# Optimization experiments

Measured on AMD Instinct MI355X. Metric: run time of the kernel, lower is better.

The kernel has to match this reference:

```python
import jax, jax.numpy as jnp
import numpy as np

CX, CY, FX, FY = 334.081, 169.808, 460.585, 460.268
EPS = 1e-07
T_ITER = 1000
MIN_POINTS = 5000
H, W, B = 360, 640, 2


def _point_cloud(depth_img):
    # depth_img: [C,H,W]; channel 2 if C==3 else channel 0
    depth = depth_img[2] if depth_img.shape[0] == 3 else depth_img[0]
    rows, cols = depth.shape
    c = jnp.arange(cols, dtype=depth.dtype)[None, :]
    r = jnp.arange(rows, dtype=depth.dtype)[:, None]
    valid = (depth > 0) & (depth < 65535)
    nanv = jnp.float32(jnp.nan)
    z = jnp.where(valid, depth / 1000.0, nanv)
    x = jnp.where(valid, z * (c - CX) / FX, nanv)
    y = jnp.where(valid, z * (r - CY) / FY, nanv)
    pcd = jnp.stack([x.ravel(), y.ravel(), z.ravel()], axis=1)  # [N,3]
    return pcd, valid.ravel()


def setup_inputs() -> dict:
    key = jax.random.key(0)
    k1, k2 = jax.random.split(key)
    fake = jax.random.uniform(k1, (B, 1, H, W), dtype=jnp.float32)
    real = jax.random.uniform(k2, (B, 1, H, W), dtype=jnp.float32)
    return {"fake": fake, "real": real, "epoch": 5, "show_image": 0}


def _forward(fake, real, epoch):
    real_pcd, vr = _point_cloud(real[0])
    fake_pcd, vf = _point_cloud(fake[0])
    real_pcd = real_pcd * 1000.0
    fake_pcd = fake_pcd * 1000.0
    # pcd[pcd==0] = eps  (NaN==0 is False, NaNs preserved)
    real_pcd = jnp.where(real_pcd == 0, EPS, real_pcd)
    fake_pcd = jnp.where(fake_pcd == 0, EPS, fake_pcd)

    # combined validity mask (real-valid then fake-valid filtering chain)
    m = vr & vf
    cnt = jnp.maximum(jnp.sum(m), 1)

    def sel(v, fill):
        return jnp.where(m, v, fill)

    def mrmse(a, b):
        d = sel(a, 0.0) - sel(b, 0.0)
        return jnp.sqrt(jnp.sum(d * d) / cnt)

    lossX = mrmse(real_pcd[:, 0], fake_pcd[:, 0])
    lossY = mrmse(real_pcd[:, 1], fake_pcd[:, 1])
    lossZ = mrmse(real_pcd[:, 2], fake_pcd[:, 2])
    dlog = jnp.log(jnp.abs(sel(real_pcd[:, 2], 1.0))) - jnp.log(jnp.abs(sel(fake_pcd[:, 2], 1.0)))
    RMSE_log = 10000.0 * jnp.sqrt(jnp.sum(jnp.where(m, dlog * dlog, 0.0)) / cnt)
    loss17 = RMSE_log * jnp.abs(10.0 * (3.0 - jnp.exp(lossX) - jnp.exp(lossY) - jnp.exp(lossZ)))

    # ---- batched RANSAC plane fit on normalized fake cloud ----
    nan_cloud = jnp.where(jnp.isnan(fake_pcd), 0.0, fake_pcd)
    pts = nan_cloud / jnp.max(nan_cloud)  # [N,3]
    N = pts.shape[0]
    thresh = jnp.maximum(jnp.float32(0.025 - 0.001 * epoch), jnp.float32(0.005))

    rkey = jax.random.key(42)
    idx = jax.random.randint(rkey, (T_ITER, 3), 0, N)  # 3 sample points per trial
    p = pts[idx]  # [T,3,3]
    vA = p[:, 1] - p[:, 0]
    vB = p[:, 2] - p[:, 0]
    nrm = jnp.cross(vA, vB)
    nrm = nrm / jnp.linalg.norm(nrm, axis=1, keepdims=True)  # unit normals [T,3]
    kk = -jnp.sum(nrm * p[:, 1], axis=1)  # plane offsets [T]
    dist = pts @ nrm.T + kk[None, :]  # [N,T], |n|=1 so no extra divide
    inl = jnp.abs(dist) <= thresh  # [N,T]
    counts = jnp.sum(inl, axis=0)  # [T]
    # keep first trial with strictly-largest count among counts > minPoints
    score = jnp.where(counts > MIN_POINTS, counts, -1)
    best = jnp.argmax(score)
    a, b, c, d = nrm[best, 0], nrm[best, 1], nrm[best, 2], kk[best]
    inlier_mask = inl[:, best]  # [N]

    # translation/rotation were built via torch.tensor(...) -> detached in torch
    trans = jax.lax.stop_gradient(jnp.stack([jnp.zeros(()), jnp.zeros(()), d / c]))
    n2 = a * a + b * b + c * c
    cos_t = c / jnp.sqrt(n2)
    sin_t = jnp.sqrt((a * a + b * b) / n2)
    sab = jnp.sqrt(a * a + b * b)
    u1 = b / sab
    u2 = -a / sab
    R = jnp.stack([
        jnp.stack([cos_t + u1 * u1 * (1 - cos_t), u1 * u2 * (1 - cos_t), u2 * sin_t]),
        jnp.stack([u1 * u2 * (1 - cos_t), cos_t + u2 * u2 * (1 - cos_t), -u1 * sin_t]),
        jnp.stack([-u2 * sin_t, u1 * sin_t, cos_t]),
    ])
    Rt = jax.lax.stop_gradient(R).T  # torch transposes before matmul

    plane_pts = pts + trans
    zc = (plane_pts @ Rt)[:, 2]  # rotated z for all points; inliers selected by mask
    icnt = jnp.maximum(jnp.sum(inlier_mask), 1)
    zmax = jnp.max(jnp.where(inlier_mask, zc, -jnp.inf))
    zmin = jnp.min(jnp.where(inlier_mask, zc, jnp.inf))
    below = jnp.sum(jnp.where(inlier_mask, jnp.abs(zc - zmax), 0.0)) / icnt
    above = jnp.sum(jnp.where(inlier_mask, jnp.abs(zc - zmin), 0.0)) / icnt
    above = jnp.where(above == 0, jnp.float32(1e-07), above)
    plane_mean_dist_grad = 1000.0 * (above + below)

    loss_curv = loss17 + plane_mean_dist_grad
    delta = jnp.stack([RMSE_log, lossX, lossY, lossZ, plane_mean_dist_grad, loss17])
    return delta, loss_curv


def reference(fake, real, epoch, show_image):
    del show_image  # unused in the loss math
    return _forward(fake, real, epoch)
```

## Files before the change

kernel.cpp:

```cpp
#include <hip/hip_runtime.h>

namespace {

typedef float v2f __attribute__((ext_vector_type(2)));

constexpr int kW = 640;
constexpr int kN = 230400;
constexpr unsigned kSpan = 230400u;
constexpr int kB1 = 900;
constexpr int kB3 = 1024;
constexpr int kPPB3 = 225;
constexpr int kB5 = 900;
constexpr unsigned kPoison = 0xAAAAAAAAu;

struct __align__(16) Acc {
  double lossX, lossY, lossZ, rmse_log, loss17;
  float maxv;
  unsigned selkey;
};

constexpr size_t kOffAcc     = 0;
constexpr size_t kOffC1      = 256;
constexpr size_t kOffC3      = 320;
constexpr size_t kOffC5      = 384;
constexpr size_t kOffPlanes  = 512;
constexpr size_t kOffSP      = 512 + 16384;
constexpr size_t kOffZP      = kOffSP + 43200;
constexpr size_t kOffPartial = kOffZP + 28800;
constexpr size_t kOffPts     = kOffPartial + (size_t)kB3 * 256 * 4;

__device__ __forceinline__ void ast64(unsigned long long* p, unsigned long long v) {
  __hip_atomic_store(p, v, __ATOMIC_RELAXED, __HIP_MEMORY_SCOPE_AGENT);
}
__device__ __forceinline__ unsigned long long ald64(const unsigned long long* p) {
  return __hip_atomic_load(p, __ATOMIC_RELAXED, __HIP_MEMORY_SCOPE_AGENT);
}
__device__ __forceinline__ void ast32(unsigned* p, unsigned v) {
  __hip_atomic_store(p, v, __ATOMIC_RELAXED, __HIP_MEMORY_SCOPE_AGENT);
}
__device__ __forceinline__ unsigned ald32(const unsigned* p) {
  return __hip_atomic_load(p, __ATOMIC_RELAXED, __HIP_MEMORY_SCOPE_AGENT);
}

__device__ __forceinline__ unsigned rotl32(unsigned v, int r) {
  return (v << r) | (v >> (32 - r));
}

__device__ __forceinline__ void threefry(unsigned c0, unsigned c1,
                                         unsigned& o0, unsigned& o1) {
  const unsigned ks0 = 0u, ks1 = 42u, ks2 = 0x1BD11BDAu ^ 0u ^ 42u;
  unsigned x0 = c0 + ks0, x1 = c1 + ks1;
#define TFR(r) { x0 += x1; x1 = rotl32(x1, (r)); x1 ^= x0; }
  TFR(13) TFR(15) TFR(26) TFR(6)
  x0 += ks1; x1 += ks2 + 1u;
  TFR(17) TFR(29) TFR(16) TFR(24)
  x0 += ks2; x1 += ks0 + 2u;
  TFR(13) TFR(15) TFR(26) TFR(6)
  x0 += ks0; x1 += ks1 + 3u;
  TFR(17) TFR(29) TFR(16) TFR(24)
  x0 += ks1; x1 += ks2 + 4u;
  TFR(13) TFR(15) TFR(26) TFR(6)
  x0 += ks2; x1 += ks0 + 5u;
#undef TFR
  o0 = x0; o1 = x1;
}

__device__ __forceinline__ void pix_coords(float d, int row, int col, bool& valid,
                                           float& x, float& y, float& z) {
  valid = (d > 0.0f) && (d < 65535.0f);
  float z0 = d / 1000.0f;
  float x0 = z0 * ((float)col - 334.081f) / 460.585f;
  float y0 = z0 * ((float)row - 169.808f) / 460.268f;
  x = x0 * 1000.0f;
  y = y0 * 1000.0f;
  z = z0 * 1000.0f;
  if (x == 0.0f) x = 1e-7f;
  if (y == 0.0f) y = 1e-7f;
  if (z == 0.0f) z = 1e-7f;
}

__device__ __forceinline__ void make_pt(float d, int row, int col, float maxv,
                                        float& x, float& y, float& z) {
  bool v; float a, b, c;
  pix_coords(d, row, col, v, a, b, c);
  x = (v ? a : 0.f) / maxv;
  y = (v ? b : 0.f) / maxv;
  z = (v ? c : 0.f) / maxv;
}

__device__ __forceinline__ float get_thresh(int ep) {
  return (float)fmax(0.025 - 0.001 * (double)ep, 0.005);
}

__global__ __launch_bounds__(256) void k_stats(const float* __restrict__ fake,
                                               const float* __restrict__ real,
                                               float* __restrict__ out,
                                               char* __restrict__ ws) {
  Acc* acc = (Acc*)(ws + kOffAcc);
  unsigned* ctr = (unsigned*)(ws + kOffC1);
  float4* planes = (float4*)(ws + kOffPlanes);
  unsigned long long* sp = (unsigned long long*)(ws + kOffSP);
  float4* ptsraw = (float4*)(ws + kOffPts);

  const int b = blockIdx.x, t = threadIdx.x;
  const int lane = t & 63, wid = t >> 6;

  __shared__ double sD0[4], sD1[4], sD2[4], sD3[4];
  __shared__ int sI0[4];
  __shared__ float sF0[4];
  __shared__ unsigned sArr;
  __shared__ float sMaxv;

  {
    int i = b * 256 + t;
    int row = i / kW, col = i - row * kW;
    bool vr, vf; float rx, ry, rz, fx, fy, fz;
    pix_coords(real[i], row, col, vr, rx, ry, rz);
    pix_coords(fake[i], row, col, vf, fx, fy, fz);
    ptsraw[i] = make_float4(vf ? fx : 0.f, vf ? fy : 0.f, vf ? fz : 0.f, 0.f);
    double dx2 = 0, dy2 = 0, dz2 = 0, dl2 = 0; int cc = 0;
    if (vr && vf) {
      float ddx = rx - fx, ddy = ry - fy, ddz = rz - fz;
      dx2 = (double)ddx * (double)ddx;
      dy2 = (double)ddy * (double)ddy;
      dz2 = (double)ddz * (double)ddz;
      double dl = log(fabs((double)rz)) - log(fabs((double)fz));
      dl2 = dl * dl;
      cc = 1;
    }
    float mx = vf ? fmaxf(fmaxf(fx, fy), fz) : 0.0f;
    for (int o = 32; o; o >>= 1) {
      dx2 += __shfl_down(dx2, o); dy2 += __shfl_down(dy2, o);
      dz2 += __shfl_down(dz2, o); dl2 += __shfl_down(dl2, o);
      cc += __shfl_down(cc, o);
      mx = fmaxf(mx, __shfl_down(mx, o));
    }
    if (lane == 0) { sD0[wid]=dx2; sD1[wid]=dy2; sD2[wid]=dz2; sD3[wid]=dl2;
                     sI0[wid]=cc; sF0[wid]=mx; }
    __syncthreads();
    if (t == 0) {
      unsigned long long* e = sp + (size_t)b * 6;
      ast64(e + 0, __double_as_longlong(sD0[0]+sD0[1]+sD0[2]+sD0[3]));
      ast64(e + 1, __double_as_longlong(sD1[0]+sD1[1]+sD1[2]+sD1[3]));
      ast64(e + 2, __double_as_longlong(sD2[0]+sD2[1]+sD2[2]+sD2[3]));
      ast64(e + 3, __double_as_longlong(sD3[0]+sD3[1]+sD3[2]+sD3[3]));
      ast64(e + 4, (unsigned long long)(sI0[0]+sI0[1]+sI0[2]+sI0[3]));
      float bm = fmaxf(fmaxf(sF0[0], sF0[1]), fmaxf(sF0[2], sF0[3]));
      ast64(e + 5, (unsigned long long)__float_as_uint(bm));
    }
  }
  __syncthreads();
  if (t == 0)
    sArr = __hip_atomic_fetch_add(ctr, 1u, __ATOMIC_RELAXED, __HIP_MEMORY_SCOPE_AGENT);
  __syncthreads();
  if (sArr != kPoison + (unsigned)(kB1 - 1)) return;

  {
    double gx = 0, gy = 0, gz = 0, gl = 0; int gc = 0; float gm = 0.f;
    for (int r = t; r < kB1; r += 256) {
      const unsigned long long* e = sp + (size_t)r * 6;
      gx += __longlong_as_double(ald64(e + 0));
      gy += __longlong_as_double(ald64(e + 1));
      gz += __longlong_as_double(ald64(e + 2));
      gl += __longlong_as_double(ald64(e + 3));
      gc += (int)ald64(e + 4);
      gm = fmaxf(gm, __uint_as_float((unsigned)ald64(e + 5)));
    }
    for (int o = 32; o; o >>= 1) {
      gx += __shfl_down(gx, o); gy += __shfl_down(gy, o);
      gz += __shfl_down(gz, o); gl += __shfl_down(gl, o);
      gc += __shfl_down(gc, o);
      gm = fmaxf(gm, __shfl_down(gm, o));
    }
    if (lane == 0) { sD0[wid]=gx; sD1[wid]=gy; sD2[wid]=gz; sD3[wid]=gl;
                     sI0[wid]=gc; sF0[wid]=gm; }
    __syncthreads();
    if (t == 0) {
      double SX = sD0[0]+sD0[1]+sD0[2]+sD0[3];
      double SY = sD1[0]+sD1[1]+sD1[2]+sD1[3];
      double SZ = sD2[0]+sD2[1]+sD2[2]+sD2[3];
      double SL = sD3[0]+sD3[1]+sD3[2]+sD3[3];
      int CN = sI0[0]+sI0[1]+sI0[2]+sI0[3];
      float MX = fmaxf(fmaxf(sF0[0], sF0[1]), fmaxf(sF0[2], sF0[3]));
      double cntd = (CN > 0) ? (double)CN : 1.0;
      double lossX = sqrt(SX / cntd);
      double lossY = sqrt(SY / cntd);
      double lossZ = sqrt(SZ / cntd);
      double rmse_log = 10000.0 * sqrt(SL / cntd);
      double loss17 = rmse_log * fabs(10.0 * (3.0 - exp(lossX) - exp(lossY) - exp(lossZ)));
      acc->lossX = lossX; acc->lossY = lossY; acc->lossZ = lossZ;
      acc->rmse_log = rmse_log; acc->loss17 = loss17;
      acc->maxv = MX;
      acc->selkey = 0u;
      out[0] = (float)rmse_log;
      out[1] = (float)lossX;
      out[2] = (float)lossY;
      out[3] = (float)lossZ;
      out[5] = (float)loss17;
      sMaxv = MX;
    }
    __syncthreads();
  }
  {
    float maxv = sMaxv;
#pragma unroll
    for (int j = 0; j < 4; j++) {
      int pid = t * 4 + j;
      if (pid < 1000) {
        float px[3], py[3], pz[3];
#pragma unroll
        for (int v = 0; v < 3; v++) {
          unsigned p = 3u * (unsigned)pid + (unsigned)v;
          unsigned o0, o1;
          threefry(p, p + 3000u, o0, o1);
          unsigned idx = o1 % kSpan;
          int row = (int)(idx / kW), col = (int)idx - row * kW;
          make_pt(fake[idx], row, col, maxv, px[v], py[v], pz[v]);
        }
        float ax = px[1]-px[0], ay = py[1]-py[0], az = pz[1]-pz[0];
        float bx = px[2]-px[0], by = py[2]-py[0], bz = pz[2]-pz[0];
        float nx = ay*bz - az*by;
        float ny = az*bx - ax*bz;
        float nz = ax*by - ay*bx;
        float nn = sqrtf(nx*nx + ny*ny + nz*nz);
        nx /= nn; ny /= nn; nz /= nn;
        float kk = -(nx*px[1] + ny*py[1] + nz*pz[1]);
        planes[pid] = make_float4(nx, ny, nz, kk);
      } else {
        planes[pid] = make_float4(0.f, 0.f, 0.f, 3e38f);
      }
    }
  }
}

__global__ __launch_bounds__(256) void k_count(const int* __restrict__ epoch,
                                               char* __restrict__ ws) {
  Acc* acc = (Acc*)(ws + kOffAcc);
  unsigned* ctr = (unsigned*)(ws + kOffC3);
  const float4* planes = (const float4*)(ws + kOffPlanes);
  unsigned* partial = (unsigned*)(ws + kOffPartial);
  const float4* ptsraw = (const float4*)(ws + kOffPts);

  const int b = blockIdx.x, t = threadIdx.x;
  const float th = get_thresh(*epoch);
  const float maxv = acc->maxv;

  __shared__ float4 sPts[kPPB3];
  __shared__ uint4 sAcc[16][16];
  __shared__ unsigned sArr;

  if (t < kPPB3) {
    float4 r = ptsraw[b * kPPB3 + t];
    sPts[t] = make_float4(r.x / maxv, r.y / maxv, r.z / maxv, 0.f);
  }
  float4 p0 = planes[t * 4 + 0], p1 = planes[t * 4 + 1];
  float4 p2 = planes[t * 4 + 2], p3 = planes[t * 4 + 3];
  v2f Ax = {p0.x, p1.x}, Ay = {p0.y, p1.y}, Az = {p0.z, p1.z}, Aw = {p0.w, p1.w};
  v2f Bx = {p2.x, p3.x}, By = {p2.y, p3.y}, Bz = {p2.z, p3.z}, Bw = {p2.w, p3.w};
  __syncthreads();

  int c0 = 0, c1 = 0, c2 = 0, c3 = 0;
#pragma unroll 5
  for (int s = 0; s < kPPB3; ++s) {
    float4 q = sPts[s];
    v2f qx = {q.x, q.x}, qy = {q.y, q.y}, qz = {q.z, q.z};
    v2f dA = __builtin_elementwise_fma(qx, Ax,
             __builtin_elementwise_fma(qy, Ay,
             __builtin_elementwise_fma(qz, Az, Aw)));
    v2f dB = __builtin_elementwise_fma(qx, Bx,
             __builtin_elementwise_fma(qy, By,
             __builtin_elementwise_fma(qz, Bz, Bw)));
    c0 += (fabsf(dA.x) <= th) ? 1 : 0;
    c1 += (fabsf(dA.y) <= th) ? 1 : 0;
    c2 += (fabsf(dB.x) <= th) ? 1 : 0;
    c3 += (fabsf(dB.y) <= th) ? 1 : 0;
  }
  ast32(&partial[b * 256 + t],
        (unsigned)c0 | ((unsigned)c1 << 8) | ((unsigned)c2 << 16) | ((unsigned)c3 << 24));

  __syncthreads();
  if (t == 0)
    sArr = __hip_atomic_fetch_add(ctr, 1u, __ATOMIC_RELAXED, __HIP_MEMORY_SCOPE_AGENT);
  __syncthreads();
  unsigned ret = sArr;
  if (ret < kPoison + (unsigned)(kB3 - 16)) return;

  int r = (int)(ret - (kPoison + (unsigned)(kB3 - 16)));
  if (t == 0) {
    while (ald32(ctr) != kPoison + (unsigned)kB3) __builtin_amdgcn_s_sleep(2);
  }
  __syncthreads();

  int owner = r * 16 + (t & 15);
  int chunk = t >> 4;
  unsigned s0 = 0, s1 = 0, s2 = 0, s3 = 0;
  for (int row = chunk * 64; row < chunk * 64 + 64; ++row) {
    unsigned v = ald32(&partial[row * 256 + owner]);
    s0 += v & 0xFFu; s1 += (v >> 8) & 0xFFu;
    s2 += (v >> 16) & 0xFFu; s3 += (v >> 24) & 0xFFu;
  }
  sAcc[t & 15][chunk] = make_uint4(s0, s1, s2, s3);
  __syncthreads();

  unsigned mykey = 0u;
  if (t < 16) {
    unsigned t0 = 0, t1 = 0, t2 = 0, t3 = 0;
    for (int j = 0; j < 16; ++j) {
      uint4 v = sAcc[t][j];
      t0 += v.x; t1 += v.y; t2 += v.z; t3 += v.w;
    }
    unsigned tot[4] = {t0, t1, t2, t3};
    int pbase = (r * 16 + t) * 4;
#pragma unroll
    for (int k = 0; k < 4; ++k) {
      int p = pbase + k;
      if (p < 1000) {
        int score = ((int)tot[k] > 5000) ? (int)tot[k] : -1;
        unsigned key = ((unsigned)(score + 2) << 10) | (unsigned)(1023 - p);
        mykey = key > mykey ? key : mykey;
      }
    }
  }
  for (int o = 32; o; o >>= 1) {
    unsigned other = __shfl_down(mykey, o);
    mykey = other > mykey ? other : mykey;
  }
  if (t == 0) atomicMax(&acc->selkey, mykey);
}

__global__ __launch_bounds__(256) void k_zc(const int* __restrict__ epoch,
                                            float* __restrict__ out,
                                            char* __restrict__ ws) {
  Acc* acc = (Acc*)(ws + kOffAcc);
  unsigned* ctr = (unsigned*)(ws + kOffC5);
  const float4* planes = (const float4*)(ws + kOffPlanes);
  unsigned long long* zp = (unsigned long long*)(ws + kOffZP);
  const float4* ptsraw = (const float4*)(ws + kOffPts);

  const int b = blockIdx.x, t = threadIdx.x;
  const int lane = t & 63, wid = t >> 6;
  const float th = get_thresh(*epoch);
  const float maxv = acc->maxv;

  int best = 1023 - (int)(acc->selkey & 1023u);
  float4 pl = planes[best];
  const float a = pl.x, bb = pl.y, c = pl.z, d = pl.w;
  float n2 = a * a + bb * bb + c * c;
  float cos_t = c / sqrtf(n2);
  float sin_t = sqrtf((a * a + bb * bb) / n2);
  float sab = sqrtf(a * a + bb * bb);
  float u1 = bb / sab, u2 = -a / sab;
  const float r0 = -u2 * sin_t, r1 = u1 * sin_t, r2 = cos_t, tz = d / c;

  __shared__ double sD0[4];
  __shared__ int sI0[4];
  __shared__ float sF0[4], sF1[4];
  __shared__ unsigned sArr;

  double sz = 0.0; int ic = 0; float zmx = -INFINITY, zmn = -INFINITY;
  {
    float4 rw = ptsraw[b * 256 + t];
    float qx = rw.x / maxv, qy = rw.y / maxv, qz = rw.z / maxv;
    float dist = fmaf(qx, a, fmaf(qy, bb, fmaf(qz, c, d)));
    if (fabsf(dist) <= th) {
      float zc = fmaf(qx, r0, fmaf(qy, r1, (qz + tz) * r2));
      sz = (double)zc; ic = 1; zmx = zc; zmn = -zc;
    }
  }
  for (int o = 32; o; o >>= 1) {
    sz += __shfl_down(sz, o); ic += __shfl_down(ic, o);
    zmx = fmaxf(zmx, __shfl_down(zmx, o));
    zmn = fmaxf(zmn, __shfl_down(zmn, o));
  }
  if (lane == 0) { sD0[wid] = sz; sI0[wid] = ic; sF0[wid] = zmx; sF1[wid] = zmn; }
  __syncthreads();
  if (t == 0) {
    unsigned long long* e = zp + (size_t)b * 4;
    ast64(e + 0, __double_as_longlong(sD0[0]+sD0[1]+sD0[2]+sD0[3]));
    ast64(e + 1, (unsigned long long)(sI0[0]+sI0[1]+sI0[2]+sI0[3]));
    float bmx = fmaxf(fmaxf(sF0[0], sF0[1]), fmaxf(sF0[2], sF0[3]));
    float bmn = fmaxf(fmaxf(sF1[0], sF1[1]), fmaxf(sF1[2], sF1[3]));
    ast64(e + 2, (unsigned long long)__float_as_uint(bmx) |
                 ((unsigned long long)__float_as_uint(bmn) << 32));
  }
  __syncthreads();
  if (t == 0)
    sArr = __hip_atomic_fetch_add(ctr, 1u, __ATOMIC_RELAXED, __HIP_MEMORY_SCOPE_AGENT);
  __syncthreads();
  if (sArr != kPoison + (unsigned)(kB5 - 1)) return;

  {
    double gs = 0.0; int gi = 0; float gmx = -INFINITY, gmn = -INFINITY;
    for (int r = t; r < kB5; r += 256) {
      const unsigned long long* e = zp + (size_t)r * 4;
      gs += __longlong_as_double(ald64(e + 0));
      gi += (int)ald64(e + 1);
      unsigned long long mm = ald64(e + 2);
      gmx = fmaxf(gmx, __uint_as_float((unsigned)(mm & 0xFFFFFFFFu)));
      gmn = fmaxf(gmn, __uint_as_float((unsigned)(mm >> 32)));
    }
    for (int o = 32; o; o >>= 1) {
      gs += __shfl_down(gs, o); gi += __shfl_down(gi, o);
      gmx = fmaxf(gmx, __shfl_down(gmx, o));
      gmn = fmaxf(gmn, __shfl_down(gmn, o));
    }
    if (lane == 0) { sD0[wid] = gs; sI0[wid] = gi; sF0[wid] = gmx; sF1[wid] = gmn; }
    __syncthreads();
    if (t == 0) {
      double S = sD0[0]+sD0[1]+sD0[2]+sD0[3];
      int IC = sI0[0]+sI0[1]+sI0[2]+sI0[3];
      float MX = fmaxf(fmaxf(sF0[0], sF0[1]), fmaxf(sF0[2], sF0[3]));
      float MN = fmaxf(fmaxf(sF1[0], sF1[1]), fmaxf(sF1[2], sF1[3]));
      double below = 0.0, above = 0.0;
      if (IC > 0) {
        double icd = (double)IC;
        double mean = S / icd;
        below = (double)MX - mean;
        above = mean - (double)(-MN);
      }
      if (above == 0.0) above = 1e-7;
      double pmdg = 1000.0 * (above + below);
      out[4] = (float)pmdg;
      out[6] = (float)(acc->loss17 + pmdg);
    }
  }
}

}

extern "C" void kernel_launch(void* const* d_in, const int* in_sizes, int n_in,
                              void* d_out, int out_size, void* d_ws, size_t ws_size,
                              hipStream_t stream) {
  (void)in_sizes; (void)n_in; (void)out_size; (void)ws_size;
  const float* fake = (const float*)d_in[0];
  const float* real = (const float*)d_in[1];
  const int* epoch = (const int*)d_in[2];
  float* out = (float*)d_out;
  char* ws = (char*)d_ws;

  k_stats<<<kB1, 256, 0, stream>>>(fake, real, out, ws);
  k_count<<<kB3, 256, 0, stream>>>(epoch, ws);
  k_zc<<<kB5, 256, 0, stream>>>(epoch, out, ws);
}
```

Baseline: 136.9 us.

## Fuse three kernels into one cooperative persistent kernel with spin-wait grid barriers

Replaces the three launches (stats, inlier count, z-range) with a single cooperative kernel of 512 blocks. Each block keeps its 450 points in registers and shared memory across phases instead of writing and re-reading a global point buffer. Phases are joined by atomic counters and spin-wait flags. The goal is to remove launch gaps and global round-trips. In exchange it adds serialized waits on one block building the planes and risks deadlock if the blocks are not all co-resident.

```diff
diff --git a/kernel.cpp b/kernel.cpp
--- a/kernel.cpp
+++ b/kernel.cpp
@@ -7,27 +7,23 @@
 constexpr int kW = 640;
 constexpr int kN = 230400;
 constexpr unsigned kSpan = 230400u;
-constexpr int kB1 = 900;
-constexpr int kB3 = 1024;
-constexpr int kPPB3 = 225;
-constexpr int kB5 = 900;
+constexpr int kB = 512;
+constexpr int kPPB = 450;
 constexpr unsigned kPoison = 0xAAAAAAAAu;
 
-struct __align__(16) Acc {
-  double lossX, lossY, lossZ, rmse_log, loss17;
-  float maxv;
-  unsigned selkey;
-};
-
-constexpr size_t kOffAcc     = 0;
-constexpr size_t kOffC1      = 256;
-constexpr size_t kOffC3      = 320;
-constexpr size_t kOffC5      = 384;
-constexpr size_t kOffPlanes  = 512;
-constexpr size_t kOffSP      = 512 + 16384;
-constexpr size_t kOffZP      = kOffSP + 43200;
-constexpr size_t kOffPartial = kOffZP + 28800;
-constexpr size_t kOffPts     = kOffPartial + (size_t)kB3 * 256 * 4;
+constexpr size_t kOffMaxv   = 0;
+constexpr size_t kOffLoss17 = 8;
+constexpr size_t kOffC1     = 128;
+constexpr size_t kOffF1     = 192;
+constexpr size_t kOffC2     = 256;
+constexpr size_t kOffC2b    = 320;
+constexpr size_t kOffF2     = 384;
+constexpr size_t kOffC3     = 448;
+constexpr size_t kOffSel    = 512;
+constexpr size_t kOffPlanes = 1024;
+constexpr size_t kOffSP     = 1024 + 16384;
+constexpr size_t kOffZP     = kOffSP + 24576;
+constexpr size_t kOffPart   = 131072;
 
 __device__ __forceinline__ void ast64(unsigned long long* p, unsigned long long v) {
   __hip_atomic_store(p, v, __ATOMIC_RELAXED, __HIP_MEMORY_SCOPE_AGENT);
@@ -38,10 +34,6 @@
 __device__ __forceinline__ void ast32(unsigned* p, unsigned v) {
   __hip_atomic_store(p, v, __ATOMIC_RELAXED, __HIP_MEMORY_SCOPE_AGENT);
 }
-__device__ __forceinline__ unsigned ald32(const unsigned* p) {
-  return __hip_atomic_load(p, __ATOMIC_RELAXED, __HIP_MEMORY_SCOPE_AGENT);
-}
-
 __device__ __forceinline__ unsigned rotl32(unsigned v, int r) {
   return (v << r) | (v >> (32 - r));
 }
@@ -92,43 +84,76 @@
   return (float)fmax(0.025 - 0.001 * (double)ep, 0.005);
 }
 
-__global__ __launch_bounds__(256) void k_stats(const float* __restrict__ fake,
-                                               const float* __restrict__ real,
-                                               float* __restrict__ out,
-                                               char* __restrict__ ws) {
-  Acc* acc = (Acc*)(ws + kOffAcc);
-  unsigned* ctr = (unsigned*)(ws + kOffC1);
-  float4* planes = (float4*)(ws + kOffPlanes);
+__global__ __launch_bounds__(256, 2) void k_all(const float* __restrict__ fake,
+                                                const float* __restrict__ real,
+                                                const int* __restrict__ epoch,
+                                                float* __restrict__ out,
+                                                char* __restrict__ ws) {
+  unsigned long long* wMaxv = (unsigned long long*)(ws + kOffMaxv);
+  unsigned long long* wL17 = (unsigned long long*)(ws + kOffLoss17);
+  unsigned* wC1 = (unsigned*)(ws + kOffC1);
+  unsigned* wF1 = (unsigned*)(ws + kOffF1);
+  unsigned* wC2 = (unsigned*)(ws + kOffC2);
+  unsigned* wC2b = (unsigned*)(ws + kOffC2b);
+  unsigned* wF2 = (unsigned*)(ws + kOffF2);
+  unsigned* wC3 = (unsigned*)(ws + kOffC3);
+  unsigned* wSel = (unsigned*)(ws + kOffSel);
+  unsigned long long* planes = (unsigned long long*)(ws + kOffPlanes);
   unsigned long long* sp = (unsigned long long*)(ws + kOffSP);
-  float4* ptsraw = (float4*)(ws + kOffPts);
+  unsigned long long* zp = (unsigned long long*)(ws + kOffZP);
+  unsigned long long* part = (unsigned long long*)(ws + kOffPart);
 
   const int b = blockIdx.x, t = threadIdx.x;
   const int lane = t & 63, wid = t >> 6;
-
+  const float th = get_thresh(*epoch);
+
+  __shared__ float4 sPts[kPPB];
+  __shared__ uint4 sAcc[16][16];
   __shared__ double sD0[4], sD1[4], sD2[4], sD3[4];
   __shared__ int sI0[4];
-  __shared__ float sF0[4];
-  __shared__ unsigned sArr;
-  __shared__ float sMaxv;
-
+  __shared__ float sF0[4], sF1s[4];
+  __shared__ unsigned sU;
+
+  float p0x, p0y, p0z, p1x = 0.f, p1y = 0.f, p1z = 0.f;
+  const bool has2 = (t < kPPB - 256);
   {
-    int i = b * 256 + t;
-    int row = i / kW, col = i - row * kW;
-    bool vr, vf; float rx, ry, rz, fx, fy, fz;
-    pix_coords(real[i], row, col, vr, rx, ry, rz);
-    pix_coords(fake[i], row, col, vf, fx, fy, fz);
-    ptsraw[i] = make_float4(vf ? fx : 0.f, vf ? fy : 0.f, vf ? fz : 0.f, 0.f);
-    double dx2 = 0, dy2 = 0, dz2 = 0, dl2 = 0; int cc = 0;
-    if (vr && vf) {
-      float ddx = rx - fx, ddy = ry - fy, ddz = rz - fz;
-      dx2 = (double)ddx * (double)ddx;
-      dy2 = (double)ddy * (double)ddy;
-      dz2 = (double)ddz * (double)ddz;
-      double dl = log(fabs((double)rz)) - log(fabs((double)fz));
-      dl2 = dl * dl;
-      cc = 1;
-    }
-    float mx = vf ? fmaxf(fmaxf(fx, fy), fz) : 0.0f;
+    double dx2 = 0, dy2 = 0, dz2 = 0, dl2 = 0; int cc = 0; float mx = 0.f;
+    {
+      int i = b * kPPB + t;
+      int row = i / kW, col = i - row * kW;
+      bool vr, vf; float rx, ry, rz, fx, fy, fz;
+      pix_coords(real[i], row, col, vr, rx, ry, rz);
+      pix_coords(fake[i], row, col, vf, fx, fy, fz);
+      p0x = vf ? fx : 0.f; p0y = vf ? fy : 0.f; p0z = vf ? fz : 0.f;
+      if (vr && vf) {
+        float ddx = rx - fx, ddy = ry - fy, ddz = rz - fz;
+        dx2 += (double)ddx * (double)ddx;
+        dy2 += (double)ddy * (double)ddy;
+        dz2 += (double)ddz * (double)ddz;
+        double dl = log(fabs((double)rz)) - log(fabs((double)fz));
+        dl2 += dl * dl;
+        cc++;
+      }
+      if (vf) mx = fmaxf(mx, fmaxf(fmaxf(fx, fy), fz));
+    }
+    if (has2) {
+      int i = b * kPPB + t + 256;
+      int row = i / kW, col = i - row * kW;
+      bool vr, vf; float rx, ry, rz, fx, fy, fz;
+      pix_coords(real[i], row, col, vr, rx, ry, rz);
+      pix_coords(fake[i], row, col, vf, fx, fy, fz);
+      p1x = vf ? fx : 0.f; p1y = vf ? fy : 0.f; p1z = vf ? fz : 0.f;
+      if (vr && vf) {
+        float ddx = rx - fx, ddy = ry - fy, ddz = rz - fz;
+        dx2 += (double)ddx * (double)ddx;
+        dy2 += (double)ddy * (double)ddy;
+        dz2 += (double)ddz * (double)ddz;
+        double dl = log(fabs((double)rz)) - log(fabs((double)fz));
+        dl2 += dl * dl;
+        cc++;
+      }
+      if (vf) mx = fmaxf(mx, fmaxf(fmaxf(fx, fy), fz));
+    }
     for (int o = 32; o; o >>= 1) {
       dx2 += __shfl_down(dx2, o); dy2 += __shfl_down(dy2, o);
       dz2 += __shfl_down(dz2, o); dl2 += __shfl_down(dl2, o);
@@ -151,13 +176,12 @@
   }
   __syncthreads();
   if (t == 0)
-    sArr = __hip_atomic_fetch_add(ctr, 1u, __ATOMIC_RELAXED, __HIP_MEMORY_SCOPE_AGENT);
-  __syncthreads();
-  if (sArr != kPoison + (unsigned)(kB1 - 1)) return;
-
-  {
+    sU = __hip_atomic_fetch_add(wC1, 1u, __ATOMIC_ACQ_REL, __HIP_MEMORY_SCOPE_AGENT);
+  __syncthreads();
+
+  if (sU == kPoison + (unsigned)(kB - 1)) {
     double gx = 0, gy = 0, gz = 0, gl = 0; int gc = 0; float gm = 0.f;
-    for (int r = t; r < kB1; r += 256) {
+    for (int r = t; r < kB; r += 256) {
       const unsigned long long* e = sp + (size_t)r * 6;
       gx += __longlong_as_double(ald64(e + 0));
       gy += __longlong_as_double(ald64(e + 1));
@@ -175,6 +199,7 @@
     if (lane == 0) { sD0[wid]=gx; sD1[wid]=gy; sD2[wid]=gz; sD3[wid]=gl;
                      sI0[wid]=gc; sF0[wid]=gm; }
     __syncthreads();
+    __shared__ float sMaxv;
     if (t == 0) {
       double SX = sD0[0]+sD0[1]+sD0[2]+sD0[3];
       double SY = sD1[0]+sD1[1]+sD1[2]+sD1[3];
@@ -188,80 +213,84 @@
       double lossZ = sqrt(SZ / cntd);
       double rmse_log = 10000.0 * sqrt(SL / cntd);
       double loss17 = rmse_log * fabs(10.0 * (3.0 - exp(lossX) - exp(lossY) - exp(lossZ)));
-      acc->lossX = lossX; acc->lossY = lossY; acc->lossZ = lossZ;
-      acc->rmse_log = rmse_log; acc->loss17 = loss17;
-      acc->maxv = MX;
-      acc->selkey = 0u;
       out[0] = (float)rmse_log;
       out[1] = (float)lossX;
       out[2] = (float)lossY;
       out[3] = (float)lossZ;
       out[5] = (float)loss17;
+      ast64(wMaxv, (unsigned long long)__float_as_uint(MX));
+      ast64(wL17, __double_as_longlong(loss17));
+      ast32(wSel, 0u);
       sMaxv = MX;
     }
     __syncthreads();
-  }
-  {
-    float maxv = sMaxv;
+    {
+      float maxv = sMaxv;
 #pragma unroll
-    for (int j = 0; j < 4; j++) {
-      int pid = t * 4 + j;
-      if (pid < 1000) {
-        float px[3], py[3], pz[3];
+      for (int j = 0; j < 4; j++) {
+        int pid = t * 4 + j;
+        float4 pl;
+        if (pid < 1000) {
+          float px[3], py[3], pz[3];
 #pragma unroll
-        for (int v = 0; v < 3; v++) {
-          unsigned p = 3u * (unsigned)pid + (unsigned)v;
-          unsigned o0, o1;
-          threefry(p, p + 3000u, o0, o1);
-          unsigned idx = o1 % kSpan;
-          int row = (int)(idx / kW), col = (int)idx - row * kW;
-          make_pt(fake[idx], row, col, maxv, px[v], py[v], pz[v]);
+          for (int v = 0; v < 3; v++) {
+            unsigned p = 3u * (unsigned)pid + (unsigned)v;
+            unsigned o0, o1;
+            threefry(p, p + 3000u, o0, o1);
+            unsigned idx = o1 % kSpan;
+            int row = (int)(idx / kW), col = (int)idx - row * kW;
+            make_pt(fake[idx], row, col, maxv, px[v], py[v], pz[v]);
+          }
+          float ax = px[1]-px[0], ay = py[1]-py[0], az = pz[1]-pz[0];
+          float bx = px[2]-px[0], by = py[2]-py[0], bz = pz[2]-pz[0];
+          float nx = ay*bz - az*by;
+          float ny = az*bx - ax*bz;
+          float nz = ax*by - ay*bx;
+          float nn = sqrtf(nx*nx + ny*ny + nz*nz);
+          nx /= nn; ny /= nn; nz /= nn;
+          float kk = -(nx*px[1] + ny*py[1] + nz*pz[1]);
+          pl = make_float4(nx, ny, nz, kk);
+        } else {
+          pl = make_float4(0.f, 0.f, 0.f, 3e38f);
         }
-        float ax = px[1]-px[0], ay = py[1]-py[0], az = pz[1]-pz[0];
-        float bx = px[2]-px[0], by = py[2]-py[0], bz = pz[2]-pz[0];
-        float nx = ay*bz - az*by;
-        float ny = az*bx - ax*bz;
-        float nz = ax*by - ay*bx;
-        float nn = sqrtf(nx*nx + ny*ny + nz*nz);
-        nx /= nn; ny /= nn; nz /= nn;
-        float kk = -(nx*px[1] + ny*py[1] + nz*pz[1]);
-        planes[pid] = make_float4(nx, ny, nz, kk);
-      } else {
-        planes[pid] = make_float4(0.f, 0.f, 0.f, 3e38f);
-      }
-    }
-  }
-}
-
-__global__ __launch_bounds__(256) void k_count(const int* __restrict__ epoch,
-                                               char* __restrict__ ws) {
-  Acc* acc = (Acc*)(ws + kOffAcc);
-  unsigned* ctr = (unsigned*)(ws + kOffC3);
-  const float4* planes = (const float4*)(ws + kOffPlanes);
-  unsigned* partial = (unsigned*)(ws + kOffPartial);
-  const float4* ptsraw = (const float4*)(ws + kOffPts);
-
-  const int b = blockIdx.x, t = threadIdx.x;
-  const float th = get_thresh(*epoch);
-  const float maxv = acc->maxv;
-
-  __shared__ float4 sPts[kPPB3];
-  __shared__ uint4 sAcc[16][16];
-  __shared__ unsigned sArr;
-
-  if (t < kPPB3) {
-    float4 r = ptsraw[b * kPPB3 + t];
-    sPts[t] = make_float4(r.x / maxv, r.y / maxv, r.z / maxv, 0.f);
-  }
-  float4 p0 = planes[t * 4 + 0], p1 = planes[t * 4 + 1];
-  float4 p2 = planes[t * 4 + 2], p3 = planes[t * 4 + 3];
-  v2f Ax = {p0.x, p1.x}, Ay = {p0.y, p1.y}, Az = {p0.z, p1.z}, Aw = {p0.w, p1.w};
-  v2f Bx = {p2.x, p3.x}, By = {p2.y, p3.y}, Bz = {p2.z, p3.z}, Bw = {p2.w, p3.w};
-  __syncthreads();
-
-  int c0 = 0, c1 = 0, c2 = 0, c3 = 0;
-#pragma unroll 5
-  for (int s = 0; s < kPPB3; ++s) {
+        ast64(&planes[2*pid],   (unsigned long long)__float_as_uint(pl.x) |
+                               ((unsigned long long)__float_as_uint(pl.y) << 32));
+        ast64(&planes[2*pid+1], (unsigned long long)__float_as_uint(pl.z) |
+                               ((unsigned long long)__float_as_uint(pl.w) << 32));
+      }
+    }
+    __syncthreads();
+    if (t == 0)
+      __hip_atomic_store(wF1, 1u, __ATOMIC_RELEASE, __HIP_MEMORY_SCOPE_AGENT);
+  } else {
+    if (t == 0) {
+      while (__hip_atomic_load(wF1, __ATOMIC_ACQUIRE, __HIP_MEMORY_SCOPE_AGENT) == kPoison)
+        __builtin_amdgcn_s_sleep(8);
+    }
+    __syncthreads();
+  }
+
+  const float maxv = __uint_as_float((unsigned)ald64(wMaxv));
+  sPts[t] = make_float4(p0x / maxv, p0y / maxv, p0z / maxv, 0.f);
+  if (has2) sPts[t + 256] = make_float4(p1x / maxv, p1y / maxv, p1z / maxv, 0.f);
+
+  unsigned long long pq0 = ald64(&planes[2*(t*4+0)]), pq1 = ald64(&planes[2*(t*4+0)+1]);
+  unsigned long long pq2 = ald64(&planes[2*(t*4+1)]), pq3 = ald64(&planes[2*(t*4+1)+1]);
+  unsigned long long pq4 = ald64(&planes[2*(t*4+2)]), pq5 = ald64(&planes[2*(t*4+2)+1]);
+  unsigned long long pq6 = ald64(&planes[2*(t*4+3)]), pq7 = ald64(&planes[2*(t*4+3)+1]);
+  v2f Ax = {__uint_as_float((unsigned)pq0), __uint_as_float((unsigned)pq2)};
+  v2f Ay = {__uint_as_float((unsigned)(pq0>>32)), __uint_as_float((unsigned)(pq2>>32))};
+  v2f Az = {__uint_as_float((unsigned)pq1), __uint_as_float((unsigned)pq3)};
+  v2f Aw = {__uint_as_float((unsigned)(pq1>>32)), __uint_as_float((unsigned)(pq3>>32))};
+  v2f Bx = {__uint_as_float((unsigned)pq4), __uint_as_float((unsigned)pq6)};
+  v2f By = {__uint_as_float((unsigned)(pq4>>32)), __uint_as_float((unsigned)(pq6>>32))};
+  v2f Bz = {__uint_as_float((unsigned)pq5), __uint_as_float((unsigned)pq7)};
+  v2f Bw = {__uint_as_float((unsigned)(pq5>>32)), __uint_as_float((unsigned)(pq7>>32))};
+  __syncthreads();
+
+  unsigned c0 = 0, c1 = 0, c2 = 0, c3 = 0;
+#pragma unroll 6
+  for (int s = 0; s < kPPB; ++s) {
     float4 q = sPts[s];
     v2f qx = {q.x, q.x}, qy = {q.y, q.y}, qz = {q.z, q.z};
     v2f dA = __builtin_elementwise_fma(qx, Ax,
@@ -270,129 +299,132 @@
     v2f dB = __builtin_elementwise_fma(qx, Bx,
              __builtin_elementwise_fma(qy, By,
              __builtin_elementwise_fma(qz, Bz, Bw)));
-    c0 += (fabsf(dA.x) <= th) ? 1 : 0;
-    c1 += (fabsf(dA.y) <= th) ? 1 : 0;
-    c2 += (fabsf(dB.x) <= th) ? 1 : 0;
-    c3 += (fabsf(dB.y) <= th) ? 1 : 0;
-  }
-  ast32(&partial[b * 256 + t],
-        (unsigned)c0 | ((unsigned)c1 << 8) | ((unsigned)c2 << 16) | ((unsigned)c3 << 24));
-
+    c0 += (fabsf(dA.x) <= th) ? 1u : 0u;
+    c1 += (fabsf(dA.y) <= th) ? 1u : 0u;
+    c2 += (fabsf(dB.x) <= th) ? 1u : 0u;
+    c3 += (fabsf(dB.y) <= th) ? 1u : 0u;
+  }
+  ast64(&part[(size_t)b * 256 + t],
+        ((unsigned long long)(c0 | (c1 << 16))) |
+        ((unsigned long long)(c2 | (c3 << 16)) << 32));
   __syncthreads();
   if (t == 0)
-    sArr = __hip_atomic_fetch_add(ctr, 1u, __ATOMIC_RELAXED, __HIP_MEMORY_SCOPE_AGENT);
-  __syncthreads();
-  unsigned ret = sArr;
-  if (ret < kPoison + (unsigned)(kB3 - 16)) return;
-
-  int r = (int)(ret - (kPoison + (unsigned)(kB3 - 16)));
-  if (t == 0) {
-    while (ald32(ctr) != kPoison + (unsigned)kB3) __builtin_amdgcn_s_sleep(2);
-  }
-  __syncthreads();
-
-  int owner = r * 16 + (t & 15);
-  int chunk = t >> 4;
-  unsigned s0 = 0, s1 = 0, s2 = 0, s3 = 0;
-  for (int row = chunk * 64; row < chunk * 64 + 64; ++row) {
-    unsigned v = ald32(&partial[row * 256 + owner]);
-    s0 += v & 0xFFu; s1 += (v >> 8) & 0xFFu;
-    s2 += (v >> 16) & 0xFFu; s3 += (v >> 24) & 0xFFu;
-  }
-  sAcc[t & 15][chunk] = make_uint4(s0, s1, s2, s3);
-  __syncthreads();
-
-  unsigned mykey = 0u;
-  if (t < 16) {
-    unsigned t0 = 0, t1 = 0, t2 = 0, t3 = 0;
-    for (int j = 0; j < 16; ++j) {
-      uint4 v = sAcc[t][j];
-      t0 += v.x; t1 += v.y; t2 += v.z; t3 += v.w;
-    }
-    unsigned tot[4] = {t0, t1, t2, t3};
-    int pbase = (r * 16 + t) * 4;
+    sU = __hip_atomic_fetch_add(wC2, 1u, __ATOMIC_ACQ_REL, __HIP_MEMORY_SCOPE_AGENT);
+  __syncthreads();
+  unsigned ret2 = sU;
+
+  if (ret2 >= kPoison + (unsigned)(kB - 16)) {
+    int r = (int)(ret2 - (kPoison + (unsigned)(kB - 16)));
+    if (t == 0) {
+      while (__hip_atomic_load(wC2, __ATOMIC_ACQUIRE, __HIP_MEMORY_SCOPE_AGENT)
+             != kPoison + (unsigned)kB)
+        __builtin_amdgcn_s_sleep(2);
+    }
+    __syncthreads();
+    int owner = r * 16 + (t & 15);
+    int chunk = t >> 4;
+    unsigned s0 = 0, s1 = 0, s2 = 0, s3 = 0;
+    for (int row = chunk * 32; row < chunk * 32 + 32; ++row) {
+      unsigned long long v = ald64(&part[(size_t)row * 256 + owner]);
+      s0 += (unsigned)(v & 0xFFFFu);
+      s1 += (unsigned)((v >> 16) & 0xFFFFu);
+      s2 += (unsigned)((v >> 32) & 0xFFFFu);
+      s3 += (unsigned)(v >> 48);
+    }
+    sAcc[t & 15][chunk] = make_uint4(s0, s1, s2, s3);
+    __syncthreads();
+    unsigned mykey = 0u;
+    if (t < 16) {
+      unsigned t0 = 0, t1 = 0, t2 = 0, t3 = 0;
+      for (int j = 0; j < 16; ++j) {
+        uint4 v = sAcc[t][j];
+        t0 += v.x; t1 += v.y; t2 += v.z; t3 += v.w;
+      }
+      unsigned tot[4] = {t0, t1, t2, t3};
+      int pbase = (r * 16 + t) * 4;
 #pragma unroll
-    for (int k = 0; k < 4; ++k) {
-      int p = pbase + k;
-      if (p < 1000) {
+      for (int k = 0; k < 4; ++k) {
+        int p = pbase + k;
         int score = ((int)tot[k] > 5000) ? (int)tot[k] : -1;
         unsigned key = ((unsigned)(score + 2) << 10) | (unsigned)(1023 - p);
         mykey = key > mykey ? key : mykey;
       }
     }
-  }
-  for (int o = 32; o; o >>= 1) {
-    unsigned other = __shfl_down(mykey, o);
-    mykey = other > mykey ? other : mykey;
-  }
-  if (t == 0) atomicMax(&acc->selkey, mykey);
-}
-
-__global__ __launch_bounds__(256) void k_zc(const int* __restrict__ epoch,
-                                            float* __restrict__ out,
-                                            char* __restrict__ ws) {
-  Acc* acc = (Acc*)(ws + kOffAcc);
-  unsigned* ctr = (unsigned*)(ws + kOffC5);
-  const float4* planes = (const float4*)(ws + kOffPlanes);
-  unsigned long long* zp = (unsigned long long*)(ws + kOffZP);
-  const float4* ptsraw = (const float4*)(ws + kOffPts);
-
-  const int b = blockIdx.x, t = threadIdx.x;
-  const int lane = t & 63, wid = t >> 6;
-  const float th = get_thresh(*epoch);
-  const float maxv = acc->maxv;
-
-  int best = 1023 - (int)(acc->selkey & 1023u);
-  float4 pl = planes[best];
-  const float a = pl.x, bb = pl.y, c = pl.z, d = pl.w;
-  float n2 = a * a + bb * bb + c * c;
-  float cos_t = c / sqrtf(n2);
-  float sin_t = sqrtf((a * a + bb * bb) / n2);
-  float sab = sqrtf(a * a + bb * bb);
-  float u1 = bb / sab, u2 = -a / sab;
-  const float r0 = -u2 * sin_t, r1 = u1 * sin_t, r2 = cos_t, tz = d / c;
-
-  __shared__ double sD0[4];
-  __shared__ int sI0[4];
-  __shared__ float sF0[4], sF1[4];
-  __shared__ unsigned sArr;
-
-  double sz = 0.0; int ic = 0; float zmx = -INFINITY, zmn = -INFINITY;
+    for (int o = 32; o; o >>= 1) {
+      unsigned other = __shfl_down(mykey, o);
+      mykey = other > mykey ? other : mykey;
+    }
+    if (t == 0) {
+      atomicMax(wSel, mykey);
+      unsigned d = __hip_atomic_fetch_add(wC2b, 1u, __ATOMIC_ACQ_REL,
+                                          __HIP_MEMORY_SCOPE_AGENT);
+      if (d == kPoison + 15u) {
+        unsigned fin = __hip_atomic_load(wSel, __ATOMIC_RELAXED, __HIP_MEMORY_SCOPE_AGENT);
+        __hip_atomic_store(wF2, fin, __ATOMIC_RELEASE, __HIP_MEMORY_SCOPE_AGENT);
+      }
+    }
+  }
+  if (t == 0) {
+    unsigned v;
+    while ((v = __hip_atomic_load(wF2, __ATOMIC_ACQUIRE, __HIP_MEMORY_SCOPE_AGENT))
+           == kPoison)
+      __builtin_amdgcn_s_sleep(4);
+    sU = v;
+  }
+  __syncthreads();
+
   {
-    float4 rw = ptsraw[b * 256 + t];
-    float qx = rw.x / maxv, qy = rw.y / maxv, qz = rw.z / maxv;
-    float dist = fmaf(qx, a, fmaf(qy, bb, fmaf(qz, c, d)));
-    if (fabsf(dist) <= th) {
-      float zc = fmaf(qx, r0, fmaf(qy, r1, (qz + tz) * r2));
-      sz = (double)zc; ic = 1; zmx = zc; zmn = -zc;
-    }
-  }
-  for (int o = 32; o; o >>= 1) {
-    sz += __shfl_down(sz, o); ic += __shfl_down(ic, o);
-    zmx = fmaxf(zmx, __shfl_down(zmx, o));
-    zmn = fmaxf(zmn, __shfl_down(zmn, o));
-  }
-  if (lane == 0) { sD0[wid] = sz; sI0[wid] = ic; sF0[wid] = zmx; sF1[wid] = zmn; }
-  __syncthreads();
-  if (t == 0) {
-    unsigned long long* e = zp + (size_t)b * 4;
-    ast64(e + 0, __double_as_longlong(sD0[0]+sD0[1]+sD0[2]+sD0[3]));
-    ast64(e + 1, (unsigned long long)(sI0[0]+sI0[1]+sI0[2]+sI0[3]));
-    float bmx = fmaxf(fmaxf(sF0[0], sF0[1]), fmaxf(sF0[2], sF0[3]));
-    float bmn = fmaxf(fmaxf(sF1[0], sF1[1]), fmaxf(sF1[2], sF1[3]));
-    ast64(e + 2, (unsigned long long)__float_as_uint(bmx) |
-                 ((unsigned long long)__float_as_uint(bmn) << 32));
-  }
-  __syncthreads();
-  if (t == 0)
-    sArr = __hip_atomic_fetch_add(ctr, 1u, __ATOMIC_RELAXED, __HIP_MEMORY_SCOPE_AGENT);
-  __syncthreads();
-  if (sArr != kPoison + (unsigned)(kB5 - 1)) return;
-
-  {
+    int best = 1023 - (int)(sU & 1023u);
+    unsigned long long b0 = ald64(&planes[2*best]), b1 = ald64(&planes[2*best+1]);
+    const float a = __uint_as_float((unsigned)b0);
+    const float bb = __uint_as_float((unsigned)(b0 >> 32));
+    const float c = __uint_as_float((unsigned)b1);
+    const float d = __uint_as_float((unsigned)(b1 >> 32));
+    float n2 = a * a + bb * bb + c * c;
+    float cos_t = c / sqrtf(n2);
+    float sin_t = sqrtf((a * a + bb * bb) / n2);
+    float sab = sqrtf(a * a + bb * bb);
+    float u1 = bb / sab, u2 = -a / sab;
+    const float r0 = -u2 * sin_t, r1 = u1 * sin_t, r2 = cos_t, tz = d / c;
+
+    double sz = 0.0; int ic = 0; float zmx = -INFINITY, zmn = -INFINITY;
+#pragma unroll
+    for (int h = 0; h < 2; ++h) {
+      if (h == 1 && !has2) break;
+      float4 q = sPts[t + h * 256];
+      float dist = fmaf(q.x, a, fmaf(q.y, bb, fmaf(q.z, c, d)));
+      if (fabsf(dist) <= th) {
+        float zc = fmaf(q.x, r0, fmaf(q.y, r1, (q.z + tz) * r2));
+        sz += (double)zc; ic++;
+        zmx = fmaxf(zmx, zc);
+        zmn = fmaxf(zmn, -zc);
+      }
+    }
+    for (int o = 32; o; o >>= 1) {
+      sz += __shfl_down(sz, o); ic += __shfl_down(ic, o);
+      zmx = fmaxf(zmx, __shfl_down(zmx, o));
+      zmn = fmaxf(zmn, __shfl_down(zmn, o));
+    }
+    if (lane == 0) { sD0[wid] = sz; sI0[wid] = ic; sF0[wid] = zmx; sF1s[wid] = zmn; }
+    __syncthreads();
+    if (t == 0) {
+      unsigned long long* e = zp + (size_t)b * 3;
+      ast64(e + 0, __double_as_longlong(sD0[0]+sD0[1]+sD0[2]+sD0[3]));
+      ast64(e + 1, (unsigned long long)(sI0[0]+sI0[1]+sI0[2]+sI0[3]));
+      float bmx = fmaxf(fmaxf(sF0[0], sF0[1]), fmaxf(sF0[2], sF0[3]));
+      float bmn = fmaxf(fmaxf(sF1s[0], sF1s[1]), fmaxf(sF1s[2], sF1s[3]));
+      ast64(e + 2, (unsigned long long)__float_as_uint(bmx) |
+                   ((unsigned long long)__float_as_uint(bmn) << 32));
+    }
+    __syncthreads();
+    if (t == 0)
+      sU = __hip_atomic_fetch_add(wC3, 1u, __ATOMIC_ACQ_REL, __HIP_MEMORY_SCOPE_AGENT);
+    __syncthreads();
+    if (sU != kPoison + (unsigned)(kB - 1)) return;
+
     double gs = 0.0; int gi = 0; float gmx = -INFINITY, gmn = -INFINITY;
-    for (int r = t; r < kB5; r += 256) {
-      const unsigned long long* e = zp + (size_t)r * 4;
+    for (int r = t; r < kB; r += 256) {
+      const unsigned long long* e = zp + (size_t)r * 3;
       gs += __longlong_as_double(ald64(e + 0));
       gi += (int)ald64(e + 1);
       unsigned long long mm = ald64(e + 2);
@@ -404,13 +436,13 @@
       gmx = fmaxf(gmx, __shfl_down(gmx, o));
       gmn = fmaxf(gmn, __shfl_down(gmn, o));
     }
-    if (lane == 0) { sD0[wid] = gs; sI0[wid] = gi; sF0[wid] = gmx; sF1[wid] = gmn; }
+    if (lane == 0) { sD0[wid] = gs; sI0[wid] = gi; sF0[wid] = gmx; sF1s[wid] = gmn; }
     __syncthreads();
     if (t == 0) {
       double S = sD0[0]+sD0[1]+sD0[2]+sD0[3];
       int IC = sI0[0]+sI0[1]+sI0[2]+sI0[3];
       float MX = fmaxf(fmaxf(sF0[0], sF0[1]), fmaxf(sF0[2], sF0[3]));
-      float MN = fmaxf(fmaxf(sF1[0], sF1[1]), fmaxf(sF1[2], sF1[3]));
+      float MN = fmaxf(fmaxf(sF1s[0], sF1s[1]), fmaxf(sF1s[2], sF1s[3]));
       double below = 0.0, above = 0.0;
       if (IC > 0) {
         double icd = (double)IC;
@@ -420,8 +452,9 @@
       }
       if (above == 0.0) above = 1e-7;
       double pmdg = 1000.0 * (above + below);
+      double loss17 = __longlong_as_double(ald64(wL17));
       out[4] = (float)pmdg;
-      out[6] = (float)(acc->loss17 + pmdg);
+      out[6] = (float)(loss17 + pmdg);
     }
   }
 }
@@ -438,7 +471,7 @@
   float* out = (float*)d_out;
   char* ws = (char*)d_ws;
 
-  k_stats<<<kB1, 256, 0, stream>>>(fake, real, out, ws);
-  k_count<<<kB3, 256, 0, stream>>>(epoch, ws);
-  k_zc<<<kB5, 256, 0, stream>>>(epoch, out, ws);
-}
+  void* args[] = { (void*)&fake, (void*)&real, (void*)&epoch, (void*)&out, (void*)&ws };
+  hipLaunchCooperativeKernel(reinterpret_cast<void*>(&k_all),
+                             dim3(kB), dim3(256), args, 0, stream);
+}
```

New measurement: 256.7 us. 87.5% more time.
